# Optimization experiments

Hardware: AMD Instinct MI355X
Metric: run time of the kernel (lower is better)

## Reference

```python
import jax, jax.numpy as jnp
import numpy as np

KH, KW = 2, 2  # upsampling kernel size


def setup_inputs() -> dict:
    key = jax.random.key(0)
    k1, k2, k3 = jax.random.split(key, 3)
    x = jax.random.normal(k1, (4, 128, 128, 128), dtype=jnp.float32)
    # offset conv: Conv2d(C, 2*KH*KW, 3, padding=1). Torch zero-inits it; we use
    # small random weights so offsets are small (near-duplicate upsampling).
    w_off = jax.random.normal(k2, (2 * KH * KW, 128, 3, 3), dtype=jnp.float32) * 0.01
    b_off = jax.random.normal(k3, (2 * KH * KW,), dtype=jnp.float32) * 0.01
    return {"x": x, "w_off": w_off, "b_off": b_off}


def _bilinear_sample(x, sy, sx):
    """x: (N,C,H,W); sy,sx: (N,P,H,W) float sample coords. Zero outside bounds.
    Returns (N,P,C,H,W)."""
    N, C, H, W = x.shape
    P = sy.shape[1]
    xf = x.reshape(N, C, H * W)
    y0 = jnp.floor(sy)
    x0 = jnp.floor(sx)
    wy1 = sy - y0  # weight of lower (y0+1) row
    wx1 = sx - x0

    def gather(yi, xi):
        valid = (yi >= 0) & (yi <= H - 1) & (xi >= 0) & (xi <= W - 1)
        yc = jnp.clip(yi, 0, H - 1).astype(jnp.int32)
        xc = jnp.clip(xi, 0, W - 1).astype(jnp.int32)
        idx = (yc * W + xc).reshape(N, P, 1, H * W)
        idx_b = jnp.broadcast_to(idx, (N, P, C, H * W))
        xe = jnp.broadcast_to(xf[:, None], (N, P, C, H * W))
        v = jnp.take_along_axis(xe, idx_b, axis=-1).reshape(N, P, C, H, W)
        return v * valid.astype(x.dtype).reshape(N, P, 1, H, W)

    v00 = gather(y0, x0)
    v01 = gather(y0, x0 + 1)
    v10 = gather(y0 + 1, x0)
    v11 = gather(y0 + 1, x0 + 1)
    wy1e = wy1[:, :, None]  # (N,P,1,H,W)
    wx1e = wx1[:, :, None]
    return (v00 * (1 - wy1e) * (1 - wx1e)
            + v01 * (1 - wy1e) * wx1e
            + v10 * wy1e * (1 - wx1e)
            + v11 * wy1e * wx1e)


def reference(x, w_off, b_off):
    N, C, H, W = x.shape
    # offset = offset_conv(x): 3x3 conv, padding 1 -> (N, 2*KH*KW, H, W)
    off = jax.lax.conv_general_dilated(
        x, w_off, window_strides=(1, 1), padding='SAME',
        dimension_numbers=('NCHW', 'OIHW', 'NCHW')) + b_off[None, :, None, None]
    off = off.reshape(N, KH * KW, 2, H, W)  # per position p: (dy, dx)
    dy, dx = off[:, :, 0], off[:, :, 1]
    ys = jnp.arange(H, dtype=x.dtype)[None, None, :, None]
    xs = jnp.arange(W, dtype=x.dtype)[None, None, None, :]
    samp = _bilinear_sample(x, ys + dy, xs + dx)  # (N, KH*KW, C, H, W)
    # position p = i*KW + j -> output pixel (h*KH + i, w*KW + j)
    samp = samp.reshape(N, KH, KW, C, H, W).transpose(0, 3, 4, 1, 5, 2)
    return samp.reshape(N, C, H * KH, W * KW)
```

## Files before the change

### kernel.cpp

```cpp
#include <hip/hip_runtime.h>

#define H 128
#define W 128
#define C 128
#define NB 4
#define HW (H * W)
#define PXB 32
#define NSEG (W / PXB)
#define TPX 64

__global__ __launch_bounds__(256) void transpose_nchw_nhwc(
    const float* __restrict__ x, float* __restrict__ xt) {
  __shared__ float tile[TPX][C + 1];
  const int blk = blockIdx.x;
  const int n = blk >> 8;
  const int p0 = (blk & 255) * TPX;
  const float* xn = x + (size_t)n * C * HW;
  float* xtn = xt + (size_t)n * HW * C;

  const int i = threadIdx.x & 63;
  const int c0 = threadIdx.x >> 6;
#pragma unroll
  for (int c = c0; c < C; c += 4)
    tile[i][c] = xn[(size_t)c * HW + p0 + i];
  __syncthreads();

  const int cl = threadIdx.x & 31;
  const int pr = threadIdx.x >> 5;
#pragma unroll
  for (int p = pr; p < TPX; p += 8) {
    float4 v = make_float4(tile[p][4 * cl + 0], tile[p][4 * cl + 1],
                           tile[p][4 * cl + 2], tile[p][4 * cl + 3]);
    *(float4*)(xtn + (size_t)(p0 + p) * C + 4 * cl) = v;
  }
}

__global__ __launch_bounds__(256) void prep_wt(
    const float* __restrict__ wg, float* __restrict__ wt) {
  const int i = blockIdx.x * 256 + threadIdx.x;
  const int ch = i / 72;
  const int rem = i % 72;
  const int k = rem >> 3;
  const int p = rem & 7;
  wt[i] = wg[((size_t)p * C + ch) * 9 + k];
}

__global__ __launch_bounds__(256, 4) void dcn_fused_t3(
    const float* __restrict__ xt, const float* __restrict__ wt,
    const float* __restrict__ b, float* __restrict__ out) {

  __shared__ __align__(16) float lsh[4224];
  __shared__ float loff[PXB][9];
  __shared__ int4   ltapi[PXB][4];
  __shared__ float4 ltapw[PXB][4];

  const int t = threadIdx.x;
  const int bxr = blockIdx.x;
  const int bx = ((bxr & 7) << 8) | (bxr >> 3);
  const int seg = bx & (NSEG - 1);
  const int y = (bx >> 2) & (H - 1);
  const int n = bx >> 9;
  const int x0 = seg * PXB;

  const float* xtn = xt + (size_t)n * HW * C;

  {
    const int pp = t & 15;
    const int cg = t >> 4;
    const int xb = x0 + 2 * pp;
    const int cb = cg * 8;

    int xs[4];
    float colm[4];
#pragma unroll
    for (int j = 0; j < 4; ++j) {
      int xa = xb - 1 + j;
      colm[j] = ((unsigned)xa < (unsigned)W) ? 1.f : 0.f;
      xs[j] = xa < 0 ? 0 : (xa > W - 1 ? W - 1 : xa);
    }
    int pix[3][4];
    float m[3][4];
#pragma unroll
    for (int r = 0; r < 3; ++r) {
      int yy = y + r - 1;
      float rm = ((unsigned)yy < (unsigned)H) ? 1.f : 0.f;
      int yc = yy < 0 ? 0 : (yy > H - 1 ? H - 1 : yy);
#pragma unroll
      for (int j = 0; j < 4; ++j) {
        m[r][j] = rm * colm[j];
        pix[r][j] = yc * W + xs[j];
      }
    }

    float acc[2][8];
#pragma unroll
    for (int p = 0; p < 8; ++p) { acc[0][p] = 0.f; acc[1][p] = 0.f; }

#pragma unroll
    for (int c2 = 0; c2 < 2; ++c2) {
      float xvq[3][4][4];
#pragma unroll
      for (int r = 0; r < 3; ++r) {
#pragma unroll
        for (int j = 0; j < 4; ++j) {
          float4 v = *(const float4*)(xtn + (size_t)pix[r][j] * C + cb + c2 * 4);
          const float mm = m[r][j];
          xvq[r][j][0] = v.x * mm;
          xvq[r][j][1] = v.y * mm;
          xvq[r][j][2] = v.z * mm;
          xvq[r][j][3] = v.w * mm;
        }
      }
#pragma unroll
      for (int cc = 0; cc < 4; ++cc) {
        const int ch = cb + c2 * 4 + cc;
        const float4* wv4 = (const float4*)(wt + (size_t)ch * 72);
#pragma unroll
        for (int k = 0; k < 9; ++k) {
          const int r = k / 3, kw = k % 3;
          const float4 wa = wv4[2 * k];
          const float4 wb = wv4[2 * k + 1];
          const float xl = xvq[r][kw][cc];
          const float xr = xvq[r][kw + 1][cc];
          acc[0][0] += xl * wa.x; acc[0][1] += xl * wa.y;
          acc[0][2] += xl * wa.z; acc[0][3] += xl * wa.w;
          acc[0][4] += xl * wb.x; acc[0][5] += xl * wb.y;
          acc[0][6] += xl * wb.z; acc[0][7] += xl * wb.w;
          acc[1][0] += xr * wa.x; acc[1][1] += xr * wa.y;
          acc[1][2] += xr * wa.z; acc[1][3] += xr * wa.w;
          acc[1][4] += xr * wb.x; acc[1][5] += xr * wb.y;
          acc[1][6] += xr * wb.z; acc[1][7] += xr * wb.w;
        }
      }
    }
#pragma unroll
    for (int p = 0; p < 8; ++p) {
      lsh[((size_t)cg * PXB + 2 * pp) * 8 + p] = acc[0][p];
      lsh[((size_t)cg * PXB + 2 * pp + 1) * 8 + p] = acc[1][p];
    }
  }
  __syncthreads();

  {
    const int px = t >> 3;
    const int p = t & 7;
    float s = b[p];
#pragma unroll
    for (int g = 0; g < 16; ++g) s += lsh[((size_t)g * PXB + px) * 8 + p];
    loff[px][p] = s;
  }
  __syncthreads();

  if (t < 128) {
    const int px = t >> 2;
    const int pos = t & 3;
    const int xx = x0 + px;
    float sy = (float)y + loff[px][2 * pos];
    float sx = (float)xx + loff[px][2 * pos + 1];
    float y0f = floorf(sy), x0f = floorf(sx);
    float wy1 = sy - y0f, wx1 = sx - x0f;
    float wy0 = 1.f - wy1, wx0 = 1.f - wx1;
    int iy0 = (int)y0f, ix0 = (int)x0f;
    int iy1 = iy0 + 1, ix1 = ix0 + 1;
    float vy0 = ((unsigned)iy0 < (unsigned)H) ? 1.f : 0.f;
    float vy1 = ((unsigned)iy1 < (unsigned)H) ? 1.f : 0.f;
    float vx0 = ((unsigned)ix0 < (unsigned)W) ? 1.f : 0.f;
    float vx1 = ((unsigned)ix1 < (unsigned)W) ? 1.f : 0.f;
    int cy0 = iy0 < 0 ? 0 : (iy0 > H - 1 ? H - 1 : iy0);
    int cy1 = iy1 < 0 ? 0 : (iy1 > H - 1 ? H - 1 : iy1);
    int cx0 = ix0 < 0 ? 0 : (ix0 > W - 1 ? W - 1 : ix0);
    int cx1 = ix1 < 0 ? 0 : (ix1 > W - 1 ? W - 1 : ix1);
    ltapi[px][pos] = make_int4(cy0 * W + cx0, cy0 * W + cx1,
                               cy1 * W + cx0, cy1 * W + cx1);
    ltapw[px][pos] = make_float4(wy0 * wx0 * vy0 * vx0, wy0 * wx1 * vy0 * vx1,
                                 wy1 * wx0 * vy1 * vx0, wy1 * wx1 * vy1 * vx1);
  }
  __syncthreads();

  {
    const int cq = t & 31;
    const int pg = t >> 5;
    const int spx = t & 7;
    const int cg4 = t >> 3;
    const float4* xt4 = (const float4*)xtn;
    float4* lout4 = (float4*)lsh;
    float* outn = out + (size_t)n * C * (2 * H) * (2 * W);

    for (int pass = 0; pass < 4; ++pass) {
      const int px = pass * 8 + pg;
      float4 sacc[4];
#pragma unroll
      for (int pos = 0; pos < 4; ++pos) {
        const int4 o = ltapi[px][pos];
        const float4 wv = ltapw[px][pos];
        float4 v00 = xt4[(size_t)o.x * (C / 4) + cq];
        float4 v01 = xt4[(size_t)o.y * (C / 4) + cq];
        float4 v10 = xt4[(size_t)o.z * (C / 4) + cq];
        float4 v11 = xt4[(size_t)o.w * (C / 4) + cq];
        sacc[pos].x = wv.x * v00.x + wv.y * v01.x + wv.z * v10.x + wv.w * v11.x;
        sacc[pos].y = wv.x * v00.y + wv.y * v01.y + wv.z * v10.y + wv.w * v11.y;
        sacc[pos].z = wv.x * v00.z + wv.y * v01.z + wv.z * v10.z + wv.w * v11.z;
        sacc[pos].w = wv.x * v00.w + wv.y * v01.w + wv.z * v10.w + wv.w * v11.w;
      }
      __syncthreads();
#pragma unroll
      for (int pos = 0; pos < 4; ++pos)
        lout4[(pos * 8 + pg) * 33 + cq] = sacc[pos];
      __syncthreads();

      float4 v[4];
#pragma unroll
      for (int pos = 0; pos < 4; ++pos)
        v[pos] = lout4[(pos * 8 + spx) * 33 + cg4];
      const int xg = x0 + pass * 8 + spx;
      float* obase = outn + (size_t)(2 * y) * (2 * W) + 2 * xg;
#define STORE_CH(J, CMP)                                                      \
      {                                                                       \
        float* oc = obase + (size_t)(cg4 * 4 + J) * (4 * HW);                 \
        *(float2*)oc = make_float2(v[0].CMP, v[1].CMP);                       \
        *(float2*)(oc + 2 * W) = make_float2(v[2].CMP, v[3].CMP);             \
      }
      STORE_CH(0, x) STORE_CH(1, y) STORE_CH(2, z) STORE_CH(3, w)
#undef STORE_CH
    }
  }
}

__global__ __launch_bounds__(256) void dcn_fused(
    const float* __restrict__ x, const float* __restrict__ wg,
    const float* __restrict__ b, float* __restrict__ out) {

  __shared__ float lacc[16][PXB][8];
  __shared__ float loff[PXB][9];

  const int t = threadIdx.x;
  const int bx = blockIdx.x;
  const int seg = bx & (NSEG - 1);
  const int y = (bx >> 2) & (H - 1);
  const int n = bx >> 9;
  const int x0 = seg * PXB;

  const float* xn = x + (size_t)n * C * HW;

  {
    const int pp = t & 15;
    const int cg = t >> 4;
    const int xb = x0 + 2 * pp;

    int xs[4];
    float colm[4];
#pragma unroll
    for (int j = 0; j < 4; ++j) {
      int xa = xb - 1 + j;
      colm[j] = ((unsigned)xa < (unsigned)W) ? 1.f : 0.f;
      xs[j] = xa < 0 ? 0 : (xa > W - 1 ? W - 1 : xa);
    }
    int rowo[3];
    float m[3][4];
#pragma unroll
    for (int r = 0; r < 3; ++r) {
      int yy = y + r - 1;
      float rm = ((unsigned)yy < (unsigned)H) ? 1.f : 0.f;
      int yc = yy < 0 ? 0 : (yy > H - 1 ? H - 1 : yy);
      rowo[r] = yc * W;
#pragma unroll
      for (int j = 0; j < 4; ++j) m[r][j] = rm * colm[j];
    }

    float acc[2][8];
#pragma unroll
    for (int p = 0; p < 8; ++p) { acc[0][p] = 0.f; acc[1][p] = 0.f; }

    for (int c = 0; c < 8; ++c) {
      const int ch = cg * 8 + c;
      const float* xc = xn + (size_t)ch * HW;
      float xv[3][4];
#pragma unroll
      for (int r = 0; r < 3; ++r)
#pragma unroll
        for (int j = 0; j < 4; ++j)
          xv[r][j] = xc[rowo[r] + xs[j]] * m[r][j];

      const float* wc = wg + (size_t)ch * 9;
#pragma unroll
      for (int p = 0; p < 8; ++p) {
        const float* wp = wc + (size_t)p * C * 9;
#pragma unroll
        for (int r = 0; r < 3; ++r) {
#pragma unroll
          for (int kw = 0; kw < 3; ++kw) {
            const float wv = wp[r * 3 + kw];
            acc[0][p] += xv[r][kw] * wv;
            acc[1][p] += xv[r][kw + 1] * wv;
          }
        }
      }
    }
#pragma unroll
    for (int p = 0; p < 8; ++p) {
      lacc[cg][2 * pp][p] = acc[0][p];
      lacc[cg][2 * pp + 1][p] = acc[1][p];
    }
  }
  __syncthreads();

  {
    const int px = t >> 3;
    const int p = t & 7;
    float s = b[p];
#pragma unroll
    for (int g = 0; g < 16; ++g) s += lacc[g][px][p];
    loff[px][p] = s;
  }
  __syncthreads();

  {
    const int px = t & (PXB - 1);
    const int sg = t >> 5;
    const int xx = x0 + px;

    float offv[8];
#pragma unroll
    for (int q = 0; q < 8; ++q) offv[q] = loff[px][q];

    int o00[4], o01[4], o10[4], o11[4];
    float w00[4], w01[4], w10[4], w11[4];
#pragma unroll
    for (int p = 0; p < 4; ++p) {
      float sy = (float)y + offv[2 * p];
      float sx = (float)xx + offv[2 * p + 1];
      float y0f = floorf(sy), x0f = floorf(sx);
      float wy1 = sy - y0f, wx1 = sx - x0f;
      float wy0 = 1.f - wy1, wx0 = 1.f - wx1;
      int iy0 = (int)y0f, ix0 = (int)x0f;
      int iy1 = iy0 + 1, ix1 = ix0 + 1;
      float vy0 = ((unsigned)iy0 < (unsigned)H) ? 1.f : 0.f;
      float vy1 = ((unsigned)iy1 < (unsigned)H) ? 1.f : 0.f;
      float vx0 = ((unsigned)ix0 < (unsigned)W) ? 1.f : 0.f;
      float vx1 = ((unsigned)ix1 < (unsigned)W) ? 1.f : 0.f;
      int cy0 = iy0 < 0 ? 0 : (iy0 > H - 1 ? H - 1 : iy0);
      int cy1 = iy1 < 0 ? 0 : (iy1 > H - 1 ? H - 1 : iy1);
      int cx0 = ix0 < 0 ? 0 : (ix0 > W - 1 ? W - 1 : ix0);
      int cx1 = ix1 < 0 ? 0 : (ix1 > W - 1 ? W - 1 : ix1);
      o00[p] = cy0 * W + cx0; o01[p] = cy0 * W + cx1;
      o10[p] = cy1 * W + cx0; o11[p] = cy1 * W + cx1;
      w00[p] = wy0 * wx0 * vy0 * vx0;
      w01[p] = wy0 * wx1 * vy0 * vx1;
      w10[p] = wy1 * wx0 * vy1 * vx0;
      w11[p] = wy1 * wx1 * vy1 * vx1;
    }

    float* outn = out + (size_t)n * C * (2 * H) * (2 * W);
    for (int c = sg * 16; c < sg * 16 + 16; ++c) {
      const float* xc = xn + (size_t)c * HW;
      float s[4];
#pragma unroll
      for (int p = 0; p < 4; ++p) {
        s[p] = w00[p] * xc[o00[p]] + w01[p] * xc[o01[p]] +
               w10[p] * xc[o10[p]] + w11[p] * xc[o11[p]];
      }
      float* oc = outn + (size_t)c * (2 * H) * (2 * W);
      float2* r0 = (float2*)(oc + (size_t)(2 * y) * (2 * W) + 2 * xx);
      float2* r1 = (float2*)(oc + (size_t)(2 * y + 1) * (2 * W) + 2 * xx);
      *r0 = make_float2(s[0], s[1]);
      *r1 = make_float2(s[2], s[3]);
    }
  }
}

extern "C" void kernel_launch(void* const* d_in, const int* in_sizes, int n_in,
                              void* d_out, int out_size, void* d_ws, size_t ws_size,
                              hipStream_t stream) {
  const float* x = (const float*)d_in[0];
  const float* w = (const float*)d_in[1];
  const float* b = (const float*)d_in[2];
  float* out = (float*)d_out;

  const size_t xt_bytes = (size_t)NB * HW * C * sizeof(float);
  const size_t wt_bytes = (size_t)8 * C * 9 * sizeof(float);
  dim3 grid(NB * H * NSEG), block(256);

  if (d_ws != nullptr && ws_size >= xt_bytes + wt_bytes) {
    float* xt = (float*)d_ws;
    float* wt = (float*)((char*)d_ws + xt_bytes);
    prep_wt<<<dim3(36), block, 0, stream>>>(w, wt);
    transpose_nchw_nhwc<<<dim3(NB * (HW / TPX)), block, 0, stream>>>(x, xt);
    dcn_fused_t3<<<grid, block, 0, stream>>>(xt, wt, b, out);
  } else {
    dcn_fused<<<grid, block, 0, stream>>>(x, w, b, out);
  }
}
```

Baseline: 231.5 us.

## Remap sampling threads to write float4 output rows directly, dropping LDS staging

Reassigns threads in the sampling/output phase so each thread computes two adjacent pixels for two positions in one output row. It can then emit float4 stores straight to the NCHW upsampled output, with no LDS transpose round-trip and no two __syncthreads per pass. Tap indices are pre-multiplied by C/4 so the gather inner loop skips a multiply. The cost is that each thread now gathers across 4 channels for a quarter of the 128-channel row, so the gather pattern changes. The reduced LDS buffer is still used by the earlier offset-conv stage.

```diff
diff --git a/kernel.cpp b/kernel.cpp
--- a/kernel.cpp
+++ b/kernel.cpp
@@ -45,11 +45,11 @@
   wt[i] = wg[((size_t)p * C + ch) * 9 + k];
 }
 
-__global__ __launch_bounds__(256, 4) void dcn_fused_t3(
+__global__ __launch_bounds__(256, 4) void dcn_fused_t7(
     const float* __restrict__ xt, const float* __restrict__ wt,
     const float* __restrict__ b, float* __restrict__ out) {
 
-  __shared__ __align__(16) float lsh[4224];
+  __shared__ __align__(16) float lsh[4096];
   __shared__ float loff[PXB][9];
   __shared__ int4   ltapi[PXB][4];
   __shared__ float4 ltapw[PXB][4];
@@ -170,58 +170,47 @@
     int cy1 = iy1 < 0 ? 0 : (iy1 > H - 1 ? H - 1 : iy1);
     int cx0 = ix0 < 0 ? 0 : (ix0 > W - 1 ? W - 1 : ix0);
     int cx1 = ix1 < 0 ? 0 : (ix1 > W - 1 ? W - 1 : ix1);
-    ltapi[px][pos] = make_int4(cy0 * W + cx0, cy0 * W + cx1,
-                               cy1 * W + cx0, cy1 * W + cx1);
+    ltapi[px][pos] = make_int4((cy0 * W + cx0) * (C / 4), (cy0 * W + cx1) * (C / 4),
+                               (cy1 * W + cx0) * (C / 4), (cy1 * W + cx1) * (C / 4));
     ltapw[px][pos] = make_float4(wy0 * wx0 * vy0 * vx0, wy0 * wx1 * vy0 * vx1,
                                  wy1 * wx0 * vy1 * vx0, wy1 * wx1 * vy1 * vx1);
   }
   __syncthreads();
 
   {
-    const int cq = t & 31;
-    const int pg = t >> 5;
-    const int spx = t & 7;
-    const int cg4 = t >> 3;
+    const int pair = t & 3;
+    const int q = (t >> 2) & 31;
+    const int half = t >> 7;
     const float4* xt4 = (const float4*)xtn;
-    float4* lout4 = (float4*)lsh;
-    float* outn = out + (size_t)n * C * (2 * H) * (2 * W);
-
+    float* outn = out + (size_t)n * C * 4 * HW;
+
+#pragma unroll 1
     for (int pass = 0; pass < 4; ++pass) {
-      const int px = pass * 8 + pg;
-      float4 sacc[4];
-#pragma unroll
-      for (int pos = 0; pos < 4; ++pos) {
-        const int4 o = ltapi[px][pos];
-        const float4 wv = ltapw[px][pos];
-        float4 v00 = xt4[(size_t)o.x * (C / 4) + cq];
-        float4 v01 = xt4[(size_t)o.y * (C / 4) + cq];
-        float4 v10 = xt4[(size_t)o.z * (C / 4) + cq];
-        float4 v11 = xt4[(size_t)o.w * (C / 4) + cq];
-        sacc[pos].x = wv.x * v00.x + wv.y * v01.x + wv.z * v10.x + wv.w * v11.x;
-        sacc[pos].y = wv.x * v00.y + wv.y * v01.y + wv.z * v10.y + wv.w * v11.y;
-        sacc[pos].z = wv.x * v00.z + wv.y * v01.z + wv.z * v10.z + wv.w * v11.z;
-        sacc[pos].w = wv.x * v00.w + wv.y * v01.w + wv.z * v10.w + wv.w * v11.w;
-      }
-      __syncthreads();
-#pragma unroll
-      for (int pos = 0; pos < 4; ++pos)
-        lout4[(pos * 8 + pg) * 33 + cq] = sacc[pos];
-      __syncthreads();
-
-      float4 v[4];
-#pragma unroll
-      for (int pos = 0; pos < 4; ++pos)
-        v[pos] = lout4[(pos * 8 + spx) * 33 + cg4];
-      const int xg = x0 + pass * 8 + spx;
-      float* obase = outn + (size_t)(2 * y) * (2 * W) + 2 * xg;
-#define STORE_CH(J, CMP)                                                      \
-      {                                                                       \
-        float* oc = obase + (size_t)(cg4 * 4 + J) * (4 * HW);                 \
-        *(float2*)oc = make_float2(v[0].CMP, v[1].CMP);                       \
-        *(float2*)(oc + 2 * W) = make_float2(v[2].CMP, v[3].CMP);             \
-      }
-      STORE_CH(0, x) STORE_CH(1, y) STORE_CH(2, z) STORE_CH(3, w)
-#undef STORE_CH
+      const int px0p = pass * 8 + 2 * pair;
+      float sc[2][2][4];
+#pragma unroll
+      for (int bb = 0; bb < 2; ++bb) {
+#pragma unroll
+        for (int pp2 = 0; pp2 < 2; ++pp2) {
+          const int pos = 2 * half + pp2;
+          const int4 o = ltapi[px0p + bb][pos];
+          const float4 wv = ltapw[px0p + bb][pos];
+          const float4 v00 = xt4[(size_t)o.x + q];
+          const float4 v01 = xt4[(size_t)o.y + q];
+          const float4 v10 = xt4[(size_t)o.z + q];
+          const float4 v11 = xt4[(size_t)o.w + q];
+          sc[bb][pp2][0] = wv.x * v00.x + wv.y * v01.x + wv.z * v10.x + wv.w * v11.x;
+          sc[bb][pp2][1] = wv.x * v00.y + wv.y * v01.y + wv.z * v10.y + wv.w * v11.y;
+          sc[bb][pp2][2] = wv.x * v00.z + wv.y * v01.z + wv.z * v10.z + wv.w * v11.z;
+          sc[bb][pp2][3] = wv.x * v00.w + wv.y * v01.w + wv.z * v10.w + wv.w * v11.w;
+        }
+      }
+      float* obase = outn + (size_t)(2 * y + half) * (2 * W) + 2 * (x0 + px0p);
+#pragma unroll
+      for (int j = 0; j < 4; ++j) {
+        *(float4*)(obase + (size_t)(4 * q + j) * (4 * HW)) =
+            make_float4(sc[0][0][j], sc[0][1][j], sc[1][0][j], sc[1][1][j]);
+      }
     }
   }
 }
@@ -378,15 +367,15 @@
 
   const size_t xt_bytes = (size_t)NB * HW * C * sizeof(float);
   const size_t wt_bytes = (size_t)8 * C * 9 * sizeof(float);
-  dim3 grid(NB * H * NSEG), block(256);
+  dim3 block(256);
 
   if (d_ws != nullptr && ws_size >= xt_bytes + wt_bytes) {
     float* xt = (float*)d_ws;
     float* wt = (float*)((char*)d_ws + xt_bytes);
     prep_wt<<<dim3(36), block, 0, stream>>>(w, wt);
     transpose_nchw_nhwc<<<dim3(NB * (HW / TPX)), block, 0, stream>>>(x, xt);
-    dcn_fused_t3<<<grid, block, 0, stream>>>(xt, wt, b, out);
+    dcn_fused_t7<<<dim3(NB * H * NSEG), block, 0, stream>>>(xt, wt, b, out);
   } else {
-    dcn_fused<<<grid, block, 0, stream>>>(x, w, b, out);
-  }
-}
+    dcn_fused<<<dim3(NB * H * NSEG), block, 0, stream>>>(x, w, b, out);
+  }
+}
```

Measured after the change: 308.6 us. +33.3%, slower.

## Restructure offset conv: stage weights in LDS, 4-pixel register tiles per thread

Applied to the files above, without the earlier changes.

The offset-conv stage now copies a re-laid-out weight tensor (36 KB) into shared memory once per block. Each thread owns 4 input channels and 4 adjacent pixels, loading 6 taps per row and reusing them across pixels, instead of 8 channels and 2 pixels with weights read from global memory. Partial sums are reduced across 32 channel groups through a padded LDS buffer that is reused for the tap tables and output staging. The aim is fewer redundant global weight and input loads per FMA. The cost is much more LDS per block, which may reduce occupancy, and a longer cross-thread reduction.

```diff
diff --git a/kernel.cpp b/kernel.cpp
--- a/kernel.cpp
+++ b/kernel.cpp
@@ -35,24 +35,23 @@
   }
 }
 
-__global__ __launch_bounds__(256) void prep_wt(
-    const float* __restrict__ wg, float* __restrict__ wt) {
+__global__ __launch_bounds__(256) void prep_wt2(
+    const float* __restrict__ wg, float* __restrict__ wt2) {
   const int i = blockIdx.x * 256 + threadIdx.x;
-  const int ch = i / 72;
-  const int rem = i % 72;
-  const int k = rem >> 3;
-  const int p = rem & 7;
-  wt[i] = wg[((size_t)p * C + ch) * 9 + k];
-}
-
-__global__ __launch_bounds__(256, 4) void dcn_fused_t3(
-    const float* __restrict__ xt, const float* __restrict__ wt,
+  const int c = i & 3;
+  int r = i >> 2;
+  const int q = r & 31; r >>= 5;
+  const int g = r & 1;  r >>= 1;
+  const int k = r % 9;
+  const int ch = r / 9;
+  wt2[i] = wg[((size_t)(4 * g + c) * C + 4 * q + ch) * 9 + k];
+}
+
+__global__ __launch_bounds__(256, 4) void dcn_fused_t8(
+    const float* __restrict__ xt, const float* __restrict__ wt2,
     const float* __restrict__ b, float* __restrict__ out) {
 
-  __shared__ __align__(16) float lsh[4224];
-  __shared__ float loff[PXB][9];
-  __shared__ int4   ltapi[PXB][4];
-  __shared__ float4 ltapw[PXB][4];
+  __shared__ __align__(16) float4 lsh4[2304];
 
   const int t = threadIdx.x;
   const int bxr = blockIdx.x;
@@ -65,98 +64,99 @@
   const float* xtn = xt + (size_t)n * HW * C;
 
   {
-    const int pp = t & 15;
-    const int cg = t >> 4;
-    const int xb = x0 + 2 * pp;
-    const int cb = cg * 8;
-
-    int xs[4];
-    float colm[4];
-#pragma unroll
-    for (int j = 0; j < 4; ++j) {
+    const float4* w4 = (const float4*)wt2;
+#pragma unroll
+    for (int i = 0; i < 9; ++i)
+      lsh4[t + 256 * i] = w4[t + 256 * i];
+  }
+  __syncthreads();
+
+  {
+    const int q = t & 31;
+    const int s = t >> 5;
+    const int xb = x0 + 4 * s;
+
+    int xs[6];
+    float colm[6];
+#pragma unroll
+    for (int j = 0; j < 6; ++j) {
       int xa = xb - 1 + j;
       colm[j] = ((unsigned)xa < (unsigned)W) ? 1.f : 0.f;
       xs[j] = xa < 0 ? 0 : (xa > W - 1 ? W - 1 : xa);
     }
-    int pix[3][4];
-    float m[3][4];
+
+    float acc[4][8];
+#pragma unroll
+    for (int px = 0; px < 4; ++px)
+#pragma unroll
+      for (int p = 0; p < 8; ++p) acc[px][p] = 0.f;
+
 #pragma unroll
     for (int r = 0; r < 3; ++r) {
       int yy = y + r - 1;
-      float rm = ((unsigned)yy < (unsigned)H) ? 1.f : 0.f;
+      float rmv = ((unsigned)yy < (unsigned)H) ? 1.f : 0.f;
       int yc = yy < 0 ? 0 : (yy > H - 1 ? H - 1 : yy);
-#pragma unroll
-      for (int j = 0; j < 4; ++j) {
-        m[r][j] = rm * colm[j];
-        pix[r][j] = yc * W + xs[j];
-      }
-    }
-
-    float acc[2][8];
-#pragma unroll
-    for (int p = 0; p < 8; ++p) { acc[0][p] = 0.f; acc[1][p] = 0.f; }
-
-#pragma unroll
-    for (int c2 = 0; c2 < 2; ++c2) {
-      float xvq[3][4][4];
-#pragma unroll
-      for (int r = 0; r < 3; ++r) {
-#pragma unroll
-        for (int j = 0; j < 4; ++j) {
-          float4 v = *(const float4*)(xtn + (size_t)pix[r][j] * C + cb + c2 * 4);
-          const float mm = m[r][j];
-          xvq[r][j][0] = v.x * mm;
-          xvq[r][j][1] = v.y * mm;
-          xvq[r][j][2] = v.z * mm;
-          xvq[r][j][3] = v.w * mm;
+      const float* xrow = xtn + (size_t)yc * W * C + 4 * q;
+      float tap[6][4];
+#pragma unroll
+      for (int j = 0; j < 6; ++j) {
+        float4 v = *(const float4*)(xrow + (size_t)xs[j] * C);
+        const float mm = rmv * colm[j];
+        tap[j][0] = v.x * mm; tap[j][1] = v.y * mm;
+        tap[j][2] = v.z * mm; tap[j][3] = v.w * mm;
+      }
+#pragma unroll
+      for (int kw = 0; kw < 3; ++kw) {
+        const int k = 3 * r + kw;
+#pragma unroll
+        for (int ch = 0; ch < 4; ++ch) {
+          const float4 wa = lsh4[((ch * 9 + k) * 2 + 0) * 32 + q];
+          const float4 wb = lsh4[((ch * 9 + k) * 2 + 1) * 32 + q];
+#pragma unroll
+          for (int px = 0; px < 4; ++px) {
+            const float tv = tap[kw + px][ch];
+            acc[px][0] += tv * wa.x; acc[px][1] += tv * wa.y;
+            acc[px][2] += tv * wa.z; acc[px][3] += tv * wa.w;
+            acc[px][4] += tv * wb.x; acc[px][5] += tv * wb.y;
+            acc[px][6] += tv * wb.z; acc[px][7] += tv * wb.w;
+          }
         }
       }
-#pragma unroll
-      for (int cc = 0; cc < 4; ++cc) {
-        const int ch = cb + c2 * 4 + cc;
-        const float4* wv4 = (const float4*)(wt + (size_t)ch * 72);
-#pragma unroll
-        for (int k = 0; k < 9; ++k) {
-          const int r = k / 3, kw = k % 3;
-          const float4 wa = wv4[2 * k];
-          const float4 wb = wv4[2 * k + 1];
-          const float xl = xvq[r][kw][cc];
-          const float xr = xvq[r][kw + 1][cc];
-          acc[0][0] += xl * wa.x; acc[0][1] += xl * wa.y;
-          acc[0][2] += xl * wa.z; acc[0][3] += xl * wa.w;
-          acc[0][4] += xl * wb.x; acc[0][5] += xl * wb.y;
-          acc[0][6] += xl * wb.z; acc[0][7] += xl * wb.w;
-          acc[1][0] += xr * wa.x; acc[1][1] += xr * wa.y;
-          acc[1][2] += xr * wa.z; acc[1][3] += xr * wa.w;
-          acc[1][4] += xr * wb.x; acc[1][5] += xr * wb.y;
-          acc[1][6] += xr * wb.z; acc[1][7] += xr * wb.w;
-        }
-      }
-    }
-#pragma unroll
-    for (int p = 0; p < 8; ++p) {
-      lsh[((size_t)cg * PXB + 2 * pp) * 8 + p] = acc[0][p];
-      lsh[((size_t)cg * PXB + 2 * pp + 1) * 8 + p] = acc[1][p];
-    }
-  }
-  __syncthreads();
-
-  {
+    }
+
+    __syncthreads();
+    float* accl = (float*)lsh4;
+    const int base = 257 * q + 32 * s;
+#pragma unroll
+    for (int px = 0; px < 4; ++px)
+#pragma unroll
+      for (int p = 0; p < 8; ++p)
+        accl[base + 8 * px + p] = acc[px][p];
+  }
+  __syncthreads();
+
+  {
+    const float* accl = (const float*)lsh4;
+    float* loff = (float*)(lsh4 + 2056);
     const int px = t >> 3;
     const int p = t & 7;
+    const int c = 32 * (px >> 2) + 8 * (px & 3) + p;
     float s = b[p];
 #pragma unroll
-    for (int g = 0; g < 16; ++g) s += lsh[((size_t)g * PXB + px) * 8 + p];
-    loff[px][p] = s;
+    for (int q = 0; q < 32; ++q) s += accl[257 * q + c];
+    loff[px * 9 + p] = s;
   }
   __syncthreads();
 
   if (t < 128) {
+    const float* loff = (const float*)(lsh4 + 2056);
+    int4* ltapi = (int4*)lsh4;
+    float4* ltapw = lsh4 + 128;
     const int px = t >> 2;
     const int pos = t & 3;
     const int xx = x0 + px;
-    float sy = (float)y + loff[px][2 * pos];
-    float sx = (float)xx + loff[px][2 * pos + 1];
+    float sy = (float)y + loff[px * 9 + 2 * pos];
+    float sx = (float)xx + loff[px * 9 + 2 * pos + 1];
     float y0f = floorf(sy), x0f = floorf(sx);
     float wy1 = sy - y0f, wx1 = sx - x0f;
     float wy0 = 1.f - wy1, wx0 = 1.f - wx1;
@@ -170,20 +170,22 @@
     int cy1 = iy1 < 0 ? 0 : (iy1 > H - 1 ? H - 1 : iy1);
     int cx0 = ix0 < 0 ? 0 : (ix0 > W - 1 ? W - 1 : ix0);
     int cx1 = ix1 < 0 ? 0 : (ix1 > W - 1 ? W - 1 : ix1);
-    ltapi[px][pos] = make_int4(cy0 * W + cx0, cy0 * W + cx1,
-                               cy1 * W + cx0, cy1 * W + cx1);
-    ltapw[px][pos] = make_float4(wy0 * wx0 * vy0 * vx0, wy0 * wx1 * vy0 * vx1,
-                                 wy1 * wx0 * vy1 * vx0, wy1 * wx1 * vy1 * vx1);
-  }
-  __syncthreads();
-
-  {
+    ltapi[px * 4 + pos] = make_int4(cy0 * W + cx0, cy0 * W + cx1,
+                                    cy1 * W + cx0, cy1 * W + cx1);
+    ltapw[px * 4 + pos] = make_float4(wy0 * wx0 * vy0 * vx0, wy0 * wx1 * vy0 * vx1,
+                                      wy1 * wx0 * vy1 * vx0, wy1 * wx1 * vy1 * vx1);
+  }
+  __syncthreads();
+
+  {
+    const int4* ltapi = (const int4*)lsh4;
+    const float4* ltapw = lsh4 + 128;
+    float4* lout4 = lsh4 + 256;
     const int cq = t & 31;
     const int pg = t >> 5;
     const int spx = t & 7;
     const int cg4 = t >> 3;
     const float4* xt4 = (const float4*)xtn;
-    float4* lout4 = (float4*)lsh;
     float* outn = out + (size_t)n * C * (2 * H) * (2 * W);
 
     for (int pass = 0; pass < 4; ++pass) {
@@ -191,8 +193,8 @@
       float4 sacc[4];
 #pragma unroll
       for (int pos = 0; pos < 4; ++pos) {
-        const int4 o = ltapi[px][pos];
-        const float4 wv = ltapw[px][pos];
+        const int4 o = ltapi[px * 4 + pos];
+        const float4 wv = ltapw[px * 4 + pos];
         float4 v00 = xt4[(size_t)o.x * (C / 4) + cq];
         float4 v01 = xt4[(size_t)o.y * (C / 4) + cq];
         float4 v10 = xt4[(size_t)o.z * (C / 4) + cq];
@@ -377,16 +379,16 @@
   float* out = (float*)d_out;
 
   const size_t xt_bytes = (size_t)NB * HW * C * sizeof(float);
-  const size_t wt_bytes = (size_t)8 * C * 9 * sizeof(float);
-  dim3 grid(NB * H * NSEG), block(256);
+  const size_t wt_bytes = (size_t)9216 * sizeof(float);
+  dim3 block(256);
 
   if (d_ws != nullptr && ws_size >= xt_bytes + wt_bytes) {
     float* xt = (float*)d_ws;
-    float* wt = (float*)((char*)d_ws + xt_bytes);
-    prep_wt<<<dim3(36), block, 0, stream>>>(w, wt);
+    float* wt2 = (float*)((char*)d_ws + xt_bytes);
+    prep_wt2<<<dim3(36), block, 0, stream>>>(w, wt2);
     transpose_nchw_nhwc<<<dim3(NB * (HW / TPX)), block, 0, stream>>>(x, xt);
-    dcn_fused_t3<<<grid, block, 0, stream>>>(xt, wt, b, out);
+    dcn_fused_t8<<<dim3(NB * H * NSEG), block, 0, stream>>>(xt, wt2, b, out);
   } else {
-    dcn_fused<<<grid, block, 0, stream>>>(x, w, b, out);
-  }
-}
+    dcn_fused<<<dim3(NB * H * NSEG), block, 0, stream>>>(x, w, b, out);
+  }
+}
```

After: 209.8 us. 1.1x faster.
